# Kernel optimization log

Measured on AMD Instinct MI355X. Metric: run time of the kernel, lower is better.

The kernel has to match this reference:

```python
import jax, jax.numpy as jnp
import numpy as np

B, C, H, W, N = 2, 64, 512, 512, 150000


def setup_inputs() -> dict:
    key = jax.random.key(0)
    k = jax.random.split(key, 6)
    return {
        "before_pseudoimages": jax.random.normal(k[0], (B, C, H, W), jnp.float32),
        "after_pseudoimages": jax.random.normal(k[1], (B, C, H, W), jnp.float32),
        "point_offsets": jax.random.normal(k[2], (B, N, 3), jnp.float32),
        "voxel_coords": jax.random.randint(k[3], (B, N, 3), 0, 512, jnp.int32),
        "W1": jax.random.normal(k[4], (131, 32), jnp.float32) * 0.08,
        "b1": jnp.zeros((32,), jnp.float32),
        "W2": jax.random.normal(k[5], (32, 3), jnp.float32) * 0.18,
        "b2": jnp.zeros((3,), jnp.float32),
    }


def reference(before_pseudoimages, after_pseudoimages, point_offsets, voxel_coords,
              W1, b1, W2, b2):
    # voxel_coords[..., 0] is the Z index, asserted == 0 in the original; unused.
    ys = voxel_coords[..., 1]  # [B, N]
    xs = voxel_coords[..., 2]  # [B, N]

    def gather(img, y, x):
        # img: [C, H, W] -> gathered [N, C]  (matches pseudoimage[:, y, x].T)
        return img[:, y, x].T

    before_vecs = jax.vmap(gather)(before_pseudoimages, ys, xs)  # [B, N, C]
    after_vecs = jax.vmap(gather)(after_pseudoimages, ys, xs)    # [B, N, C]
    feats = jnp.concatenate([before_vecs, after_vecs, point_offsets], axis=-1)  # [B, N, 131]

    h = jax.nn.gelu(jnp.einsum("bnf,fh->bnh", feats, W1) + b1, approximate=False)
    flow = jnp.einsum("bnh,ho->bno", h, W2) + b2  # [B, N, 3]
    return flow
```

## Files before the change

### kernel.cpp

```cpp
#include <hip/hip_runtime.h>
#include <math.h>

#define NCH   64
#define IMW   512
#define NPTS  150000
#define TOTAL (2 * NPTS)
#define IMHW  (512 * 512)
#define HID   32
#define NBINS 32768

#define WL_B1 4192
#define WL_W2 4224
#define WL_B2 4320
#define WL_SZ 4324


__global__ __launch_bounds__(256) void hist_kernel(const int* __restrict__ coords,
                                                   int* __restrict__ hist) {
    int gid = blockIdx.x * blockDim.x + threadIdx.x;
    if (gid >= TOTAL) return;
    const int y = coords[gid * 3 + 1];
    const int x = coords[gid * 3 + 2];
    const int b = (gid >= NPTS) ? 1 : 0;
    const int key = (b << 14) | (y << 5) | (x >> 4);
    atomicAdd(&hist[key], 1);
}

__global__ __launch_bounds__(1024) void scan_kernel(const int* __restrict__ hist,
                                                    int* __restrict__ binPos) {
    __shared__ int lds[1024];
    const int t = threadIdx.x;
    const int base = t * 32;
    int loc[32];
    int s = 0;
    #pragma unroll
    for (int i = 0; i < 32; ++i) { loc[i] = s; s += hist[base + i]; }
    lds[t] = s;
    __syncthreads();
    for (int d = 1; d < 1024; d <<= 1) {
        int v = lds[t];
        int add = (t >= d) ? lds[t - d] : 0;
        __syncthreads();
        lds[t] = v + add;
        __syncthreads();
    }
    const int excl = lds[t] - s;
    #pragma unroll
    for (int i = 0; i < 32; ++i) binPos[base + i] = excl + loc[i];
}

__global__ __launch_bounds__(256) void scatter_kernel(const int* __restrict__ coords,
                                                      int* __restrict__ binPos,
                                                      int* __restrict__ perm) {
    int gid = blockIdx.x * blockDim.x + threadIdx.x;
    if (gid >= TOTAL) return;
    const int y = coords[gid * 3 + 1];
    const int x = coords[gid * 3 + 2];
    const int b = (gid >= NPTS) ? 1 : 0;
    const int key = (b << 14) | (y << 5) | (x >> 4);
    const int pos = atomicAdd(&binPos[key], 1);
    perm[pos] = gid;
}


__global__ __launch_bounds__(256) void ffd_kernel(
    const float* __restrict__ before,
    const float* __restrict__ after,
    const float* __restrict__ offsets,
    const int*   __restrict__ coords,
    const float* __restrict__ W1,
    const float* __restrict__ b1,
    const float* __restrict__ W2,
    const float* __restrict__ b2,
    const int*   __restrict__ perm,
    float*       __restrict__ out)
{
    __shared__ float wl[WL_SZ];

    for (int i = threadIdx.x; i < 131 * HID; i += 256) wl[i] = W1[i];
    if (threadIdx.x < HID) wl[WL_B1 + threadIdx.x] = b1[threadIdx.x];
    if (threadIdx.x < 96)  wl[WL_W2 + threadIdx.x] = W2[threadIdx.x];
    if (threadIdx.x < 3)   wl[WL_B2 + threadIdx.x] = b2[threadIdx.x];
    __syncthreads();

    int gpt = blockIdx.x * blockDim.x + threadIdx.x;
    const bool valid = gpt < TOTAL;
    if (!valid) gpt = TOTAL - 1;

    const int pid = perm ? perm[gpt] : gpt;
    const long pbase = (long)pid * 3;

    const int y = coords[pbase + 1];
    const int x = coords[pbase + 2];
    const int b = (pid >= NPTS) ? 1 : 0;

    const long img_off = (long)b * NCH * IMHW + (long)y * IMW + x;
    const float* bp = before + img_off;
    const float* ap = after  + img_off;

    float acc[HID];
    {
        const float o0 = offsets[pbase + 0];
        const float o1 = offsets[pbase + 1];
        const float o2 = offsets[pbase + 2];
        const float* r0 = &wl[128 * HID];
        const float* r1 = &wl[129 * HID];
        const float* r2 = &wl[130 * HID];
        #pragma unroll
        for (int h = 0; h < HID; ++h)
            acc[h] = fmaf(o2, r2[h], fmaf(o1, r1[h], fmaf(o0, r0[h], wl[WL_B1 + h])));
    }

    float g[16];

    for (int cc = 0; cc < NCH; cc += 16) {
        #pragma unroll
        for (int j = 0; j < 16; ++j) g[j] = bp[(long)(cc + j) * IMHW];
        #pragma unroll
        for (int j = 0; j < 16; ++j) {
            const float* wr = &wl[(cc + j) * HID];
            #pragma unroll
            for (int h = 0; h < HID; ++h) acc[h] = fmaf(g[j], wr[h], acc[h]);
        }
    }
    for (int cc = 0; cc < NCH; cc += 16) {
        #pragma unroll
        for (int j = 0; j < 16; ++j) g[j] = ap[(long)(cc + j) * IMHW];
        #pragma unroll
        for (int j = 0; j < 16; ++j) {
            const float* wr = &wl[(64 + cc + j) * HID];
            #pragma unroll
            for (int h = 0; h < HID; ++h) acc[h] = fmaf(g[j], wr[h], acc[h]);
        }
    }

    #pragma unroll
    for (int h = 0; h < HID; ++h) {
        const float xh = acc[h];
        acc[h] = 0.5f * xh * (1.0f + erff(xh * 0.70710678118654752f));
    }

    float q0 = wl[WL_B2 + 0], q1 = wl[WL_B2 + 1], q2 = wl[WL_B2 + 2];
    #pragma unroll
    for (int h = 0; h < HID; ++h) {
        q0 = fmaf(acc[h], wl[WL_W2 + h * 3 + 0], q0);
        q1 = fmaf(acc[h], wl[WL_W2 + h * 3 + 1], q1);
        q2 = fmaf(acc[h], wl[WL_W2 + h * 3 + 2], q2);
    }

    if (valid) {
        out[pbase + 0] = q0;
        out[pbase + 1] = q1;
        out[pbase + 2] = q2;
    }
}

extern "C" void kernel_launch(void* const* d_in, const int* in_sizes, int n_in,
                              void* d_out, int out_size, void* d_ws, size_t ws_size,
                              hipStream_t stream) {
    const float* before  = (const float*)d_in[0];
    const float* after   = (const float*)d_in[1];
    const float* offsets = (const float*)d_in[2];
    const int*   coords  = (const int*)  d_in[3];
    const float* W1      = (const float*)d_in[4];
    const float* b1      = (const float*)d_in[5];
    const float* W2      = (const float*)d_in[6];
    const float* b2      = (const float*)d_in[7];
    float* out = (float*)d_out;

    const int block = 256;
    const int grid  = (TOTAL + block - 1) / block;

    const size_t need = (size_t)(2 * NBINS + TOTAL) * sizeof(int);

    if (ws_size >= need) {
        int* hist   = (int*)d_ws;
        int* binPos = hist + NBINS;
        int* perm   = binPos + NBINS;

        hipMemsetAsync(hist, 0, NBINS * sizeof(int), stream);
        hist_kernel<<<grid, block, 0, stream>>>(coords, hist);
        scan_kernel<<<1, 1024, 0, stream>>>(hist, binPos);
        scatter_kernel<<<grid, block, 0, stream>>>(coords, binPos, perm);
        ffd_kernel<<<grid, block, 0, stream>>>(before, after, offsets, coords,
                                               W1, b1, W2, b2, perm, out);
    } else {
        ffd_kernel<<<grid, block, 0, stream>>>(before, after, offsets, coords,
                                               W1, b1, W2, b2, nullptr, out);
    }
}
```

Measured before the change: 120.7 us.

## Precompute dense first-layer activations per pixel, then gather per point

Adds a dense kernel that streams both pseudoimages contiguously with float2 loads and computes the image part of the first linear layer for every pixel into a workspace buffer H. A per-point kernel then gathers a 32-float row from H, adds the offset terms, and applies GELU and the second layer. This trades the scattered channel-strided gathers and the sort pipeline for a full coalesced pass over the images plus a large intermediate write. It also requires a workspace of NPIX*32 floats, and it falls back to the old sorted path when the workspace is too small. Weights now come straight from global memory instead of LDS.

```diff
diff --git a/kernel.cpp b/kernel.cpp
--- a/kernel.cpp
+++ b/kernel.cpp
@@ -7,12 +7,116 @@
 #define TOTAL (2 * NPTS)
 #define IMHW  (512 * 512)
 #define HID   32
+#define NPIX  (2 * IMHW)
 #define NBINS 32768
 
-#define WL_B1 4192
-#define WL_W2 4224
-#define WL_B2 4320
-#define WL_SZ 4324
+
+__global__ __launch_bounds__(256) void dense_h_kernel(
+    const float* __restrict__ before,
+    const float* __restrict__ after,
+    const float* __restrict__ W1,
+    const float* __restrict__ b1,
+    float*       __restrict__ H)
+{
+    const long p0 = (long)blockIdx.x * 512 + (long)threadIdx.x * 2;
+    const int  b  = (int)(p0 >> 18);
+    const int  hw = (int)(p0 & (IMHW - 1));
+
+    const float* bp = before + (long)b * NCH * IMHW + hw;
+    const float* ap = after  + (long)b * NCH * IMHW + hw;
+
+    float a0[HID], a1[HID];
+    #pragma unroll
+    for (int h = 0; h < HID; ++h) { a0[h] = b1[h]; a1[h] = b1[h]; }
+
+    float2 g[16];
+
+    #pragma unroll
+    for (int ck = 0; ck < 4; ++ck) {
+        #pragma unroll
+        for (int j = 0; j < 16; ++j)
+            g[j] = *reinterpret_cast<const float2*>(bp + (long)(ck * 16 + j) * IMHW);
+        #pragma unroll
+        for (int j = 0; j < 16; ++j) {
+            const float* wr = W1 + (ck * 16 + j) * HID;
+            #pragma unroll
+            for (int h = 0; h < HID; ++h) {
+                a0[h] = fmaf(g[j].x, wr[h], a0[h]);
+                a1[h] = fmaf(g[j].y, wr[h], a1[h]);
+            }
+        }
+    }
+    #pragma unroll
+    for (int ck = 0; ck < 4; ++ck) {
+        #pragma unroll
+        for (int j = 0; j < 16; ++j)
+            g[j] = *reinterpret_cast<const float2*>(ap + (long)(ck * 16 + j) * IMHW);
+        #pragma unroll
+        for (int j = 0; j < 16; ++j) {
+            const float* wr = W1 + (64 + ck * 16 + j) * HID;
+            #pragma unroll
+            for (int h = 0; h < HID; ++h) {
+                a0[h] = fmaf(g[j].x, wr[h], a0[h]);
+                a1[h] = fmaf(g[j].y, wr[h], a1[h]);
+            }
+        }
+    }
+
+    float4* o0 = reinterpret_cast<float4*>(H + p0 * HID);
+    float4* o1 = reinterpret_cast<float4*>(H + (p0 + 1) * HID);
+    #pragma unroll
+    for (int q = 0; q < 8; ++q)
+        o0[q] = make_float4(a0[q*4+0], a0[q*4+1], a0[q*4+2], a0[q*4+3]);
+    #pragma unroll
+    for (int q = 0; q < 8; ++q)
+        o1[q] = make_float4(a1[q*4+0], a1[q*4+1], a1[q*4+2], a1[q*4+3]);
+}
+
+__global__ __launch_bounds__(256) void point_kernel(
+    const float* __restrict__ H,
+    const float* __restrict__ offsets,
+    const int*   __restrict__ coords,
+    const float* __restrict__ W1,
+    const float* __restrict__ W2,
+    const float* __restrict__ b2,
+    float*       __restrict__ out)
+{
+    const int gid = blockIdx.x * blockDim.x + threadIdx.x;
+    if (gid >= TOTAL) return;
+
+    const int  b     = (gid >= NPTS) ? 1 : 0;
+    const long pbase = (long)gid * 3;
+    const int  y     = coords[pbase + 1];
+    const int  x     = coords[pbase + 2];
+
+    const long pix = (long)b * IMHW + (long)y * IMW + x;
+    const float4* hp = reinterpret_cast<const float4*>(H + pix * HID);
+
+    float4 hv[8];
+    #pragma unroll
+    for (int q = 0; q < 8; ++q) hv[q] = hp[q];
+
+    const float o0 = offsets[pbase + 0];
+    const float o1 = offsets[pbase + 1];
+    const float o2 = offsets[pbase + 2];
+    const float* r0 = W1 + 128 * HID;
+    const float* r1 = W1 + 129 * HID;
+    const float* r2 = W1 + 130 * HID;
+
+    float q0 = b2[0], q1 = b2[1], q2 = b2[2];
+    #pragma unroll
+    for (int h = 0; h < HID; ++h) {
+        float v = reinterpret_cast<const float*>(hv)[h];
+        v = fmaf(o2, r2[h], fmaf(o1, r1[h], fmaf(o0, r0[h], v)));
+        v = 0.5f * v * (1.0f + erff(v * 0.70710678118654752f));
+        q0 = fmaf(v, W2[h * 3 + 0], q0);
+        q1 = fmaf(v, W2[h * 3 + 1], q1);
+        q2 = fmaf(v, W2[h * 3 + 2], q2);
+    }
+    out[pbase + 0] = q0;
+    out[pbase + 1] = q1;
+    out[pbase + 2] = q2;
+}
 
 
 __global__ __launch_bounds__(256) void hist_kernel(const int* __restrict__ coords,
@@ -22,8 +126,7 @@
     const int y = coords[gid * 3 + 1];
     const int x = coords[gid * 3 + 2];
     const int b = (gid >= NPTS) ? 1 : 0;
-    const int key = (b << 14) | (y << 5) | (x >> 4);
-    atomicAdd(&hist[key], 1);
+    atomicAdd(&hist[(b << 14) | (y << 5) | (x >> 4)], 1);
 }
 
 __global__ __launch_bounds__(1024) void scan_kernel(const int* __restrict__ hist,
@@ -57,13 +160,11 @@
     const int y = coords[gid * 3 + 1];
     const int x = coords[gid * 3 + 2];
     const int b = (gid >= NPTS) ? 1 : 0;
-    const int key = (b << 14) | (y << 5) | (x >> 4);
-    const int pos = atomicAdd(&binPos[key], 1);
+    const int pos = atomicAdd(&binPos[(b << 14) | (y << 5) | (x >> 4)], 1);
     perm[pos] = gid;
 }
 
-
-__global__ __launch_bounds__(256) void ffd_kernel(
+__global__ __launch_bounds__(256) void ffd_gather_kernel(
     const float* __restrict__ before,
     const float* __restrict__ after,
     const float* __restrict__ offsets,
@@ -75,21 +176,12 @@
     const int*   __restrict__ perm,
     float*       __restrict__ out)
 {
-    __shared__ float wl[WL_SZ];
-
-    for (int i = threadIdx.x; i < 131 * HID; i += 256) wl[i] = W1[i];
-    if (threadIdx.x < HID) wl[WL_B1 + threadIdx.x] = b1[threadIdx.x];
-    if (threadIdx.x < 96)  wl[WL_W2 + threadIdx.x] = W2[threadIdx.x];
-    if (threadIdx.x < 3)   wl[WL_B2 + threadIdx.x] = b2[threadIdx.x];
-    __syncthreads();
-
     int gpt = blockIdx.x * blockDim.x + threadIdx.x;
     const bool valid = gpt < TOTAL;
     if (!valid) gpt = TOTAL - 1;
 
     const int pid = perm ? perm[gpt] : gpt;
     const long pbase = (long)pid * 3;
-
     const int y = coords[pbase + 1];
     const int x = coords[pbase + 2];
     const int b = (pid >= NPTS) ? 1 : 0;
@@ -103,22 +195,21 @@
         const float o0 = offsets[pbase + 0];
         const float o1 = offsets[pbase + 1];
         const float o2 = offsets[pbase + 2];
-        const float* r0 = &wl[128 * HID];
-        const float* r1 = &wl[129 * HID];
-        const float* r2 = &wl[130 * HID];
+        const float* r0 = W1 + 128 * HID;
+        const float* r1 = W1 + 129 * HID;
+        const float* r2 = W1 + 130 * HID;
         #pragma unroll
         for (int h = 0; h < HID; ++h)
-            acc[h] = fmaf(o2, r2[h], fmaf(o1, r1[h], fmaf(o0, r0[h], wl[WL_B1 + h])));
+            acc[h] = fmaf(o2, r2[h], fmaf(o1, r1[h], fmaf(o0, r0[h], b1[h])));
     }
 
     float g[16];
-
     for (int cc = 0; cc < NCH; cc += 16) {
         #pragma unroll
         for (int j = 0; j < 16; ++j) g[j] = bp[(long)(cc + j) * IMHW];
         #pragma unroll
         for (int j = 0; j < 16; ++j) {
-            const float* wr = &wl[(cc + j) * HID];
+            const float* wr = W1 + (cc + j) * HID;
             #pragma unroll
             for (int h = 0; h < HID; ++h) acc[h] = fmaf(g[j], wr[h], acc[h]);
         }
@@ -128,7 +219,7 @@
         for (int j = 0; j < 16; ++j) g[j] = ap[(long)(cc + j) * IMHW];
         #pragma unroll
         for (int j = 0; j < 16; ++j) {
-            const float* wr = &wl[(64 + cc + j) * HID];
+            const float* wr = W1 + (64 + cc + j) * HID;
             #pragma unroll
             for (int h = 0; h < HID; ++h) acc[h] = fmaf(g[j], wr[h], acc[h]);
         }
@@ -139,15 +230,13 @@
         const float xh = acc[h];
         acc[h] = 0.5f * xh * (1.0f + erff(xh * 0.70710678118654752f));
     }
-
-    float q0 = wl[WL_B2 + 0], q1 = wl[WL_B2 + 1], q2 = wl[WL_B2 + 2];
+    float q0 = b2[0], q1 = b2[1], q2 = b2[2];
     #pragma unroll
     for (int h = 0; h < HID; ++h) {
-        q0 = fmaf(acc[h], wl[WL_W2 + h * 3 + 0], q0);
-        q1 = fmaf(acc[h], wl[WL_W2 + h * 3 + 1], q1);
-        q2 = fmaf(acc[h], wl[WL_W2 + h * 3 + 2], q2);
-    }
-
+        q0 = fmaf(acc[h], W2[h * 3 + 0], q0);
+        q1 = fmaf(acc[h], W2[h * 3 + 1], q1);
+        q2 = fmaf(acc[h], W2[h * 3 + 2], q2);
+    }
     if (valid) {
         out[pbase + 0] = q0;
         out[pbase + 1] = q1;
@@ -169,23 +258,31 @@
     float* out = (float*)d_out;
 
     const int block = 256;
-    const int grid  = (TOTAL + block - 1) / block;
-
-    const size_t need = (size_t)(2 * NBINS + TOTAL) * sizeof(int);
-
-    if (ws_size >= need) {
+
+    const size_t needH = (size_t)NPIX * HID * sizeof(float);
+
+    if (ws_size >= needH) {
+        float* H = (float*)d_ws;
+        dense_h_kernel<<<NPIX / 512, block, 0, stream>>>(before, after, W1, b1, H);
+        point_kernel<<<(TOTAL + block - 1) / block, block, 0, stream>>>(
+            H, offsets, coords, W1, W2, b2, out);
+        return;
+    }
+
+    const int grid = (TOTAL + block - 1) / block;
+    const size_t needS = (size_t)(2 * NBINS + TOTAL) * sizeof(int);
+    if (ws_size >= needS) {
         int* hist   = (int*)d_ws;
         int* binPos = hist + NBINS;
         int* perm   = binPos + NBINS;
-
         hipMemsetAsync(hist, 0, NBINS * sizeof(int), stream);
         hist_kernel<<<grid, block, 0, stream>>>(coords, hist);
         scan_kernel<<<1, 1024, 0, stream>>>(hist, binPos);
         scatter_kernel<<<grid, block, 0, stream>>>(coords, binPos, perm);
-        ffd_kernel<<<grid, block, 0, stream>>>(before, after, offsets, coords,
-                                               W1, b1, W2, b2, perm, out);
+        ffd_gather_kernel<<<grid, block, 0, stream>>>(before, after, offsets, coords,
+                                                      W1, b1, W2, b2, perm, out);
     } else {
-        ffd_kernel<<<grid, block, 0, stream>>>(before, after, offsets, coords,
-                                               W1, b1, W2, b2, nullptr, out);
-    }
-}
+        ffd_gather_kernel<<<grid, block, 0, stream>>>(before, after, offsets, coords,
+                                                      W1, b1, W2, b2, nullptr, out);
+    }
+}
```

Result: slower. 129.4 us (+7.2%).
